# Kernel optimization log

Hardware: AMD Instinct MI355X
Metric: run time of the kernel (lower is better)

Reference implementation:

```python
import jax, jax.numpy as jnp
import numpy as np

D, H = 256, 4            # model dim, num heads
HD = D // H              # head dim (even, needed by rotate_half)
B, N, M, NS = 2, 6, 512, 512  # batch, views, t keypoints, s keypoints
EPS = 1e-5


def _linear(x, w, b):
    return x @ w + b


def _ln(x, g, b):
    mu = x.mean(-1, keepdims=True)
    var = ((x - mu) ** 2).mean(-1, keepdims=True)
    return (x - mu) * jax.lax.rsqrt(var + EPS) * g + b


def _ffn(x, f1w, f1b, lng, lnb, f2w, f2b):
    # Linear(2d,2d) -> LayerNorm -> exact GELU -> Linear(2d,d)
    h = jax.nn.gelu(_ln(_linear(x, f1w, f1b), lng, lnb), approximate=False)
    return _linear(h, f2w, f2b)


def _rotate_half(x):
    # pairs (x0,x1) -> (-x1, x0), interleaved
    return jnp.stack((-x[..., 1::2], x[..., 0::2]), axis=-1).reshape(x.shape)


def _rope(freqs, t):
    return t * freqs[0] + _rotate_half(t) * freqs[1]


def _attn(q, k, v):
    sim = jnp.einsum('...id,...jd->...ij', q, k) * (q.shape[-1] ** -0.5)
    return jnp.einsum('...ij,...jd->...id', jax.nn.softmax(sim, axis=-1), v)


def _self_block(x, enc, qkv_w, qkv_b, out_w, out_b, *ffn_p):
    b, n_img, m, d = x.shape
    enc = jnp.swapaxes(enc, 2, 3)  # encoding.dim()==6 path
    qkv = _linear(x, qkv_w, qkv_b).reshape(b, n_img, m, H, HD, 3)
    qkv = jnp.swapaxes(qkv, -4, -3)  # [b,N,H,m,hd,3]
    q, k, v = qkv[..., 0], qkv[..., 1], qkv[..., 2]
    ctx = _attn(_rope(enc, q), _rope(enc, k), v)  # [b,N,H,m,hd]
    msg = _linear(jnp.swapaxes(ctx, -3, -2).reshape(b, n_img, m, d), out_w, out_b)
    return x + _ffn(jnp.concatenate([x, msg], -1), *ffn_p)


def _t2t_block(t, qkv_w, qkv_b, out_w, out_b, *ffn_p):
    t2 = jnp.swapaxes(t, 1, 2)  # [b,m,N,d]
    b, m, n_img, d = t2.shape
    qkv = _linear(t2, qkv_w, qkv_b).reshape(b, m, n_img, H, HD, 3)
    qkv = jnp.swapaxes(qkv, 3, 2)  # [b,m,H,N,hd,3]
    q, k, v = qkv[..., 0], qkv[..., 1], qkv[..., 2]
    ctx = _attn(q, k, v)  # [b,m,H,N,hd]
    msg = _linear(jnp.swapaxes(ctx, 3, 2).reshape(b, m, n_img, d), out_w, out_b)
    return jnp.swapaxes(t2 + _ffn(jnp.concatenate([t2, msg], -1), *ffn_p), 1, 2)


def _s2s_block(s, q_enc, k_enc, qkv_w, qkv_b, out_w, out_b, *ffn_p):
    b, n_img, n, d = s.shape
    qkv = _linear(s, qkv_w, qkv_b).reshape(b, n_img, n, H, HD, 3)
    qkv = jnp.swapaxes(jnp.swapaxes(qkv, -4, -3), -5, -4)  # [b,H,N,n,hd,3]
    q, k, v = qkv[..., 0], qkv[..., 1], qkv[..., 2]
    # expand queries across all views, RoPE per (i,j) view pair
    q = jnp.broadcast_to(q[:, :, None], (b, H, n_img, n_img, n, HD))
    q = _rope(q_enc, q).reshape(b, H, n_img, n_img * n, HD)
    k = _rope(k_enc, k)
    ctx = _attn(q, k, v).reshape(b, H, n_img, n_img, n, HD)
    # drop diagonal (i==j) entries exactly like boolean-mask indexing in torch
    off = np.nonzero(~np.eye(n_img, dtype=bool).ravel())[0]
    ctx = ctx.reshape(b, H, n_img * n_img, n, HD)[:, :, off]
    ctx = ctx.reshape(b, H, n_img - 1, n_img, n, HD).mean(2)  # [b,H,N,n,hd]
    ctx = jnp.swapaxes(jnp.swapaxes(ctx, 1, 2), 2, 3).reshape(b, n_img, n, d)
    msg = _linear(ctx, out_w, out_b)
    return s + _ffn(jnp.concatenate([s, msg], -1), *ffn_p)


def _cross_block(d0, d1, q_w, q_b, kv_w, kv_b, out_w, out_b, *ffn_p):
    b, n_img, m, d = d0.shape
    m1 = d1.shape[2]
    q = jnp.swapaxes(_linear(d0, q_w, q_b).reshape(b, n_img, m, H, HD), 2, 3)
    kv = jnp.swapaxes(_linear(d1, kv_w, kv_b).reshape(b, n_img, m1, H, HD, 2), 2, 3)
    ctx = _attn(q, kv[..., 0], kv[..., 1])  # [b,N,H,m,hd]
    msg = _linear(jnp.swapaxes(ctx, 2, 3).reshape(b, n_img, m, d), out_w, out_b)
    return d0 + _ffn(jnp.concatenate([d0, msg], -1), *ffn_p)


def setup_inputs() -> dict:
    key = jax.random.key(0)
    ks = iter(jax.random.split(key, 80))
    f32 = jnp.float32

    def lin(din, dout):
        return (jax.random.normal(next(ks), (din, dout), f32) * (din ** -0.5),
                jnp.zeros((dout,), f32))

    inp = {}
    inp['t_desc'] = jax.random.normal(next(ks), (B, N, M, D), f32)
    inp['s_desc'] = jax.random.normal(next(ks), (B, N, NS, D), f32)
    inp['t_encoding'] = jax.random.normal(next(ks), (2, 1, 1, N, M, HD), f32)
    inp['s_encoding'] = jax.random.normal(next(ks), (2, 1, 1, N, NS, HD), f32)
    inp['q_encoding'] = jax.random.normal(next(ks), (2, 1, 1, N, N, 1, HD), f32)
    inp['k_encoding'] = jax.random.normal(next(ks), (2, 1, 1, N, NS, HD), f32)
    for pre in ('sa', 'ss', 'tt'):
        inp[pre + '_qkv_w'], inp[pre + '_qkv_b'] = lin(D, 3 * D)
        inp[pre + '_out_w'], inp[pre + '_out_b'] = lin(D, D)
        inp[pre + '_f1_w'], inp[pre + '_f1_b'] = lin(2 * D, 2 * D)
        inp[pre + '_ln_g'] = jnp.ones((2 * D,), f32)
        inp[pre + '_ln_b'] = jnp.zeros((2 * D,), f32)
        inp[pre + '_f2_w'], inp[pre + '_f2_b'] = lin(2 * D, D)
    inp['ca_q_w'], inp['ca_q_b'] = lin(D, D)
    inp['ca_kv_w'], inp['ca_kv_b'] = lin(D, 2 * D)
    inp['ca_out_w'], inp['ca_out_b'] = lin(D, D)
    inp['ca_f1_w'], inp['ca_f1_b'] = lin(2 * D, 2 * D)
    inp['ca_ln_g'] = jnp.ones((2 * D,), f32)
    inp['ca_ln_b'] = jnp.zeros((2 * D,), f32)
    inp['ca_f2_w'], inp['ca_f2_b'] = lin(2 * D, D)
    inp['cf_w1'], inp['cf_b1'] = lin(D, D)
    inp['cf_w2'], inp['cf_b2'] = lin(D, 1)
    return inp


def reference(t_desc, s_desc, t_encoding, s_encoding, q_encoding, k_encoding,
              sa_qkv_w, sa_qkv_b, sa_out_w, sa_out_b, sa_f1_w, sa_f1_b, sa_ln_g, sa_ln_b, sa_f2_w, sa_f2_b,
              ss_qkv_w, ss_qkv_b, ss_out_w, ss_out_b, ss_f1_w, ss_f1_b, ss_ln_g, ss_ln_b, ss_f2_w, ss_f2_b,
              tt_qkv_w, tt_qkv_b, tt_out_w, tt_out_b, tt_f1_w, tt_f1_b, tt_ln_g, tt_ln_b, tt_f2_w, tt_f2_b,
              ca_q_w, ca_q_b, ca_kv_w, ca_kv_b, ca_out_w, ca_out_b, ca_f1_w, ca_f1_b, ca_ln_g, ca_ln_b, ca_f2_w, ca_f2_b,
              cf_w1, cf_b1, cf_w2, cf_b2):
    sa = (sa_qkv_w, sa_qkv_b, sa_out_w, sa_out_b, sa_f1_w, sa_f1_b, sa_ln_g, sa_ln_b, sa_f2_w, sa_f2_b)
    t = _self_block(t_desc, t_encoding, *sa)   # shared SelfBlock weights
    s = _self_block(s_desc, s_encoding, *sa)
    t = _t2t_block(t, tt_qkv_w, tt_qkv_b, tt_out_w, tt_out_b, tt_f1_w, tt_f1_b, tt_ln_g, tt_ln_b, tt_f2_w, tt_f2_b)
    s = _s2s_block(s, q_encoding, k_encoding, ss_qkv_w, ss_qkv_b, ss_out_w, ss_out_b, ss_f1_w, ss_f1_b, ss_ln_g, ss_ln_b, ss_f2_w, ss_f2_b)
    ca = (ca_q_w, ca_q_b, ca_kv_w, ca_kv_b, ca_out_w, ca_out_b, ca_f1_w, ca_f1_b, ca_ln_g, ca_ln_b, ca_f2_w, ca_f2_b)
    t2 = _cross_block(t, s, *ca)               # shared CrossBlock weights
    s2 = _cross_block(s, t, *ca)
    conf = _linear(jax.nn.relu(_linear(jax.lax.stop_gradient(s), cf_w1, cf_b1)), cf_w2, cf_b2)[..., 0]
    return t2, s2, conf
```

## Files before the change

### kernel.cpp

```cpp
#include <hip/hip_runtime.h>
#include <hip/hip_bf16.h>
#include <math.h>

constexpr int kD   = 256;
constexpr int kH   = 4;
constexpr int kHD  = 64;
constexpr int kB   = 2;
constexpr int kN   = 6;
constexpr int kM   = 512;
constexpr int kRowsH = kB*kN*kM;
constexpr int kRows  = 2*kRowsH;
constexpr int kGrpH  = kB*kN*kH;
constexpr int kGrp   = 2*kGrpH;
constexpr size_t kTOK = (size_t)kRowsH*kD;
constexpr size_t kEncSlab = (size_t)kN*kM*kHD;
constexpr size_t kQEncSlab = (size_t)kN*kN*kHD;
constexpr float kL2E = 1.4426950408889634f;

typedef unsigned short u16;
typedef __attribute__((ext_vector_type(8))) short s16x8;
typedef __attribute__((ext_vector_type(4))) float f32x4;

__device__ __forceinline__ float wred_sum(float v){
  #pragma unroll
  for (int m=32;m>0;m>>=1) v += __shfl_xor(v, m, 64);
  return v;
}
__device__ __forceinline__ u16 f2b(float x){
  union { float f; unsigned u; } a; a.f = x;
  unsigned r = a.u + 0x7fffu + ((a.u >> 16) & 1u);
  return (u16)(r >> 16);
}
__device__ __forceinline__ float b2f(u16 x){
  union { unsigned u; float f; } a; a.u = ((unsigned)x) << 16;
  return a.f;
}
__device__ __forceinline__ unsigned pk2(float lo, float hi){
  union { __hip_bfloat162 h2; unsigned u; } c;
  c.h2 = __float22bfloat162_rn(make_float2(lo, hi));
  return c.u;
}

struct WtDesc { const float* W; u16* Wt; int K; int N; int ntiles; };
struct WtTable { WtDesc d[18]; };

__global__ __launch_bounds__(256) void wtcast_k(WtTable tab)
{
  int t = blockIdx.x, mi = 0;
  while (t >= tab.d[mi].ntiles) { t -= tab.d[mi].ntiles; ++mi; }
  const float* W = tab.d[mi].W;
  u16* Wt = tab.d[mi].Wt;
  const int K = tab.d[mi].K, N = tab.d[mi].N;
  const int ktn = K >> 5;
  const int nt = t / ktn, kt = t % ktn;
  const int n0 = nt*128, k0 = kt*32;
  u16* dst = Wt + (size_t)t*4096;
  #pragma unroll
  for (int s = 0; s < 2; ++s) {
    const int idx0 = (s*256 + (int)threadIdx.x)*8;
    const int ar = idx0 >> 5;
    const int w8 = (idx0 >> 3) & 3;
    const int sw = (ar >> 1) & 3;
    const int kk = k0 + ((w8 ^ sw) << 3);
    const int n  = n0 + ar;
    union { u16 u[8]; s16x8 v; } o;
    #pragma unroll
    for (int e = 0; e < 8; ++e)
      o.u[e] = f2b(W[(size_t)(kk + e)*N + n]);
    *(s16x8*)(dst + idx0) = o.v;
  }
}

template<bool A1B, bool A2B, bool CB>
__global__ __launch_bounds__(256) void mmad_k(
    const void* __restrict__ A1a, const void* __restrict__ A1b,
    const void* __restrict__ A2a, const void* __restrict__ A2b, int K1,
    const u16* __restrict__ Wa, const u16* __restrict__ Wb,
    const float* __restrict__ bia, const float* __restrict__ bib,
    const float* __restrict__ bi2a, const float* __restrict__ bi2b, int Ns,
    const float* __restrict__ Ra, const float* __restrict__ Rb,
    void* __restrict__ Cp, int N, int K, int Mh, int doRelu)
{
  __shared__ u16 As[128*32];
  __shared__ u16 Bs[128*32];
  const int tid = threadIdx.x;
  const int lane = tid & 63, w = tid >> 6;
  const int gx = gridDim.x;
  const int nblk = gx * gridDim.y;
  int flat = blockIdx.y*gx + blockIdx.x;
  if (!(nblk & 7)) flat = (flat & 7)*(nblk >> 3) + (flat >> 3);
  const int bxx = flat % gx, byy = flat / gx;
  const int row0 = byy*128, col0 = bxx*128;
  const bool sec = (row0 >= Mh);
  const int lr0 = sec ? row0 - Mh : row0;
  const void* A1 = sec ? A1b : A1a;
  const void* A2 = sec ? A2b : A2a;
  const u16* Wt  = sec ? Wb : Wa;
  const float* bias  = sec ? bib : bia;
  const float* bias2 = sec ? bi2b : bi2a;
  const float* R = sec ? Rb : Ra;
  const int wr = (w >> 1)*64, wc = (w & 1)*64;
// ... 140 lines not shown
    vs[il][c] = base[c*3+2];
  }
  __syncthreads();
  #pragma unroll 4
  for (int rr = 0; rr < 16; ++rr) {
    const int cc = rr*4 + t4;
    Vt[((size_t)g*kHD + cc)*kM + i0 + c] = vs[c][cc];
  }
}

__global__ __launch_bounds__(256) void prep_cross_k(
    const u16* __restrict__ qkvC, u16* __restrict__ Kb, u16* __restrict__ Vt)
{
  __shared__ u16 vs[64][66];
  const int g = blockIdx.x >> 3, i0 = (blockIdx.x & 7)*64;
  const int h = g & 3, bn = g >> 2;
  const int src = (bn < 12) ? bn + 12 : bn - 12;
  const int c = threadIdx.x & 63, t4 = threadIdx.x >> 6;
  #pragma unroll 4
  for (int rr = 0; rr < 16; ++rr) {
    const int il = rr*4 + t4, i = i0 + il;
    const u16* base = qkvC + ((size_t)src*kM + i)*768 + 256 + h*128;
    Kb[((size_t)g*kM + i)*kHD + c] = f2b(b2f(base[c*2]) * 0.125f);
    vs[il][c] = base[c*2+1];
  }
  __syncthreads();
  #pragma unroll 4
  for (int rr = 0; rr < 16; ++rr) {
    const int cc = rr*4 + t4;
    Vt[((size_t)g*kHD + cc)*kM + i0 + c] = vs[c][cc];
  }
}

__device__ __forceinline__ f32x4 vmax4(f32x4 a, f32x4 b){
  f32x4 r;
  r[0]=fmaxf(a[0],b[0]); r[1]=fmaxf(a[1],b[1]);
  r[2]=fmaxf(a[2],b[2]); r[3]=fmaxf(a[3],b[3]);
  return r;
}

__device__ __forceinline__ void attn_seg(
    const u16* __restrict__ Kg, const u16* __restrict__ Vg,
    s16x8 qf0, s16x8 qf1, int k0, int qr, int hi,
    f32x4 acc[4], float& m, float& l, bool first)
{
  const bool subhi = (hi & 1);
  const bool up = (hi >= 2);
  f32x4 st[16];
  #pragma unroll
  for (int t2 = 0; t2 < 16; ++t2) {
    const u16* kp = Kg + ((size_t)(k0 + t2*16 + qr))*kHD + hi*8;
    s16x8 a0 = *(const s16x8*)(kp);
    s16x8 a1 = *(const s16x8*)(kp + 32);
    f32x4 z = {0.f, 0.f, 0.f, 0.f};
    z = __builtin_amdgcn_mfma_f32_16x16x32_bf16(a0, qf0, z, 0, 0, 0);
    z = __builtin_amdgcn_mfma_f32_16x16x32_bf16(a1, qf1, z, 0, 0, 0);
    st[t2] = z;
  }
  f32x4 t8[8];
  #pragma unroll
  for (int i = 0; i < 8; ++i) t8[i] = vmax4(st[2*i], st[2*i+1]);
  #pragma unroll
  for (int i = 0; i < 4; ++i) t8[i] = vmax4(t8[i], t8[i+4]);
  t8[0] = vmax4(vmax4(t8[0], t8[1]), vmax4(t8[2], t8[3]));
  float mloc = fmaxf(fmaxf(t8[0][0], t8[0][1]), fmaxf(t8[0][2], t8[0][3]));
  mloc = fmaxf(mloc, __shfl_xor(mloc, 16));
  mloc = fmaxf(mloc, __shfl_xor(mloc, 32));
  if (first) {
    m = mloc;
  } else if (__any(mloc > m)) {
    const float mn = fmaxf(m, mloc);
    const float r = exp2f((m - mn)*kL2E);
    m = mn;
    l *= r;
    const float rr0 = __shfl(r, hi*4+0), rr1 = __shfl(r, hi*4+1);
    const float rr2 = __shfl(r, hi*4+2), rr3 = __shfl(r, hi*4+3);
    #pragma unroll
    for (int db = 0; db < 4; ++db) {
      acc[db][0] *= rr0; acc[db][1] *= rr1; acc[db][2] *= rr2; acc[db][3] *= rr3;
    }
  }
  const float mk = m * kL2E;
  #pragma unroll
  for (int t2 = 0; t2 < 16; ++t2)
    #pragma unroll
    for (int i = 0; i < 4; ++i)
      st[t2][i] = exp2f(st[t2][i]*kL2E - mk);
  {
    f32x4 s8[8];
    #pragma unroll
    for (int i = 0; i < 8; ++i) s8[i] = st[2*i] + st[2*i+1];
    #pragma unroll
    for (int i = 0; i < 4; ++i) s8[i] = s8[i] + s8[i+4];
    f32x4 s1 = (s8[0] + s8[1]) + (s8[2] + s8[3]);
    l += (s1[0] + s1[1]) + (s1[2] + s1[3]);
  }
  #pragma unroll
  for (int j = 0; j < 8; ++j) {
    const unsigned c00 = pk2(st[2*j][0],   st[2*j][1]);
    const unsigned c01 = pk2(st[2*j][2],   st[2*j][3]);
    const unsigned c10 = pk2(st[2*j+1][0], st[2*j+1][1]);
    const unsigned c11 = pk2(st[2*j+1][2], st[2*j+1][3]);
    const unsigned c00x = __shfl_xor((int)c00, 32), c10x = __shfl_xor((int)c10, 32);
    const unsigned c01x = __shfl_xor((int)c01, 32), c11x = __shfl_xor((int)c11, 32);
    const unsigned E = up ? c10x : c00, F = up ? c10 : c00x;
    const unsigned G = up ? c11x : c01, H = up ? c11 : c01x;
    const unsigned Ex = __shfl_xor((int)E, 16), Fx = __shfl_xor((int)F, 16);
    const unsigned Gx = __shfl_xor((int)G, 16), Hx = __shfl_xor((int)H, 16);
    union { unsigned w[4]; s16x8 v; } pa;
    pa.w[0] = subhi ? Fx : E;
    pa.w[1] = subhi ? Hx : G;
    pa.w[2] = subhi ? F  : Ex;
    pa.w[3] = subhi ? H  : Gx;
    #pragma unroll
    for (int db = 0; db < 4; ++db) {
      const u16* vp = Vg + ((size_t)(db*16 + qr))*kM + k0 + j*32 + hi*8;
      const s16x8 vf = *(const s16x8*)(vp);
      acc[db] = __builtin_amdgcn_mfma_f32_16x16x32_bf16(pa.v, vf, acc[db], 0, 0, 0);
    }
  }
}

__device__ __forceinline__ void attn_512(
    const u16* __restrict__ Kg, const u16* __restrict__ Vg,
    s16x8 qf0, s16x8 qf1, int qr, int hi, f32x4 acc[4], float& m, float& l)
{
  attn_seg(Kg, Vg, qf0, qf1, 0,   qr, hi, acc, m, l, true);
  attn_seg(Kg, Vg, qf0, qf1, 256, qr, hi, acc, m, l, false);
}

template<int CROSSQ>
__global__ __launch_bounds__(256) void attn_mm_k(
    const u16* __restrict__ Qb, const u16* __restrict__ Kb,
    const u16* __restrict__ Vt, u16* __restrict__ ctx)
{
  const int w = threadIdx.x >> 6, lane = threadIdx.x & 63;
  const int bij = (blockIdx.x & 7)*96 + (blockIdx.x >> 3);
  const int g = bij >> 3, qblk = bij & 7;
  const int h = g & 3, bn = g >> 2;
  const int q0 = qblk*64 + w*16;
  const int qr = lane & 15, hi = lane >> 4;

  s16x8 qf0, qf1;
  if (CROSSQ) {
    const u16* qp = Qb + ((size_t)(bn*kM + q0 + qr))*768 + h*kHD + hi*8;
    qf0 = *(const s16x8*)(qp); qf1 = *(const s16x8*)(qp + 32);
  } else {
    const u16* qp = Qb + ((size_t)g*kM + q0 + qr)*kHD + hi*8;
    qf0 = *(const s16x8*)(qp); qf1 = *(const s16x8*)(qp + 32);
  }

  const u16* Kg = Kb + (size_t)g*kM*kHD;
  const u16* Vg = Vt + (size_t)g*kHD*kM;
  f32x4 acc[4] = {};
  float m = -1e30f, l = 0.f;
  attn_512(Kg, Vg, qf0, qf1, qr, hi, acc, m, l);

  l += __shfl_xor(l, 16); l += __shfl_xor(l, 32);
  const float li = 1.f/l;
  const float l0 = __shfl(li, hi*4+0), l1 = __shfl(li, hi*4+1);
  const float l2 = __shfl(li, hi*4+2), l3 = __shfl(li, hi*4+3);
  #pragma unroll
  for (int db = 0; db < 4; ++db) {
    const size_t base = ((size_t)(bn*kM + q0 + hi*4))*kD + h*kHD + db*16 + qr;
    ctx[base + 0*kD] = f2b(acc[db][0]*l0);
    ctx[base + 1*kD] = f2b(acc[db][1]*l1);
    ctx[base + 2*kD] = f2b(acc[db][2]*l2);
    ctx[base + 3*kD] = f2b(acc[db][3]*l3);
  }
}

__device__ __forceinline__ void rope4(const f32x4 x, const f32x4 e0, const f32x4 e1, float o[4])
{
  o[0] = x[0]*e0[0] - x[1]*e1[0];
  o[1] = x[1]*e0[1] + x[0]*e1[1];
  o[2] = x[2]*e0[2] - x[3]*e1[2];
  o[3] = x[3]*e0[3] + x[2]*e1[3];
}

__global__ __launch_bounds__(256) void attn_s2s_k(
    const float* __restrict__ Qraw, const u16* __restrict__ Kb,
    const u16* __restrict__ Vt, const float* __restrict__ qenc,
    u16* __restrict__ ctx5)
{
  const int w = threadIdx.x >> 6, lane = threadIdx.x & 63;
  const int bij = (blockIdx.x & 7)*120 + (blockIdx.x >> 3);
  const int bh = bij / 120;
  const int rest = bij % 120;
  const int col = rest / 20;
  const int rem = rest % 20;
  const int qblk = rem / 5, split = rem % 5;
  const int q0 = qblk*128 + w*32;
  const int qr = lane & 15, hi = lane >> 4;
  const bool subhi = (hi & 1), up = (hi >= 2);

  const int e  = split*6 + col;
  const int iv = e/5;
  const int j0 = e%5;
  const int jv = j0 + (j0 >= iv ? 1 : 0);

  s16x8 qf0[2], qf1[2];
  #pragma unroll
  for (int f = 0; f < 2; ++f) {
    const float* qp = Qraw + ((size_t)(bh*kN + jv)*kM + q0 + f*16 + qr)*kHD + hi*8;
    const float* ep = qenc + ((size_t)(iv*kN + jv))*kHD + hi*8;
    union { u16 u[8]; s16x8 v; } A, B;
    float o[4];
    rope4(*(const f32x4*)(qp),   *(const f32x4*)(ep),   *(const f32x4*)(ep+kQEncSlab), o);
    #pragma unroll
    for (int j = 0; j < 4; ++j) A.u[j] = f2b(o[j]*0.125f);
    rope4(*(const f32x4*)(qp+4), *(const f32x4*)(ep+4), *(const f32x4*)(ep+kQEncSlab+4), o);
    #pragma unroll
    for (int j = 0; j < 4; ++j) A.u[4+j] = f2b(o[j]*0.125f);
    rope4(*(const f32x4*)(qp+32), *(const f32x4*)(ep+32), *(const f32x4*)(ep+kQEncSlab+32), o);
    #pragma unroll
    for (int j = 0; j < 4; ++j) B.u[j] = f2b(o[j]*0.125f);
    rope4(*(const f32x4*)(qp+36), *(const f32x4*)(ep+36), *(const f32x4*)(ep+kQEncSlab+36), o);
    #pragma unroll
    for (int j = 0; j < 4; ++j) B.u[4+j] = f2b(o[j]*0.125f);
    qf0[f] = A.v; qf1[f] = B.v;
  }

  const int g2 = bh*kN + iv;
  const u16* Kg = Kb + (size_t)g2*kM*kHD;
  const u16* Vg = Vt + (size_t)g2*kHD*kM;
  f32x4 acc[2][4] = {};
  float m[2] = {-1e30f, -1e30f}, l[2] = {0.f, 0.f};

  for (int kc = 0; kc < 16; ++kc) {
    const int k0 = kc*32;
    s16x8 a0[2], a1[2];
    #pragma unroll
    for (int t = 0; t < 2; ++t) {
      const u16* kp = Kg + ((size_t)(k0 + t*16 + qr))*kHD + hi*8;
      a0[t] = *(const s16x8*)(kp);
      a1[t] = *(const s16x8*)(kp + 32);
    }
    s16x8 pa[2];
    #pragma unroll
    for (int f = 0; f < 2; ++f) {
      f32x4 st[2];
      #pragma unroll
      for (int t = 0; t < 2; ++t) {
        f32x4 z = {0.f, 0.f, 0.f, 0.f};
        z = __builtin_amdgcn_mfma_f32_16x16x32_bf16(a0[t], qf0[f], z, 0, 0, 0);
        z = __builtin_amdgcn_mfma_f32_16x16x32_bf16(a1[t], qf1[f], z, 0, 0, 0);
        st[t] = z;
      }
      float mloc = fmaxf(fmaxf(fmaxf(st[0][0], st[0][1]), fmaxf(st[0][2], st[0][3])),
                         fmaxf(fmaxf(st[1][0], st[1][1]), fmaxf(st[1][2], st[1][3])));
      mloc = fmaxf(mloc, __shfl_xor(mloc, 16));
      mloc = fmaxf(mloc, __shfl_xor(mloc, 32));
      if (!__all(mloc - m[f] <= 8.f)) {
        const float mn = fmaxf(m[f], mloc);
        const float r = exp2f((m[f] - mn)*kL2E);
        m[f] = mn;
        l[f] *= r;
        const float rr0 = __shfl(r, hi*4+0), rr1 = __shfl(r, hi*4+1);
// ... 9 lines not shown
      for (int t = 0; t < 2; ++t)
        #pragma unroll
        for (int j = 0; j < 4; ++j) {
          const float pv = exp2f((st[t][j] - m[f])*kL2E);
          p[t*4+j] = pv; ls += pv;
        }
      l[f] += ls;
      const unsigned c00 = pk2(p[0], p[1]);
      const unsigned c01 = pk2(p[2], p[3]);
      const unsigned c10 = pk2(p[4], p[5]);
      const unsigned c11 = pk2(p[6], p[7]);
      const unsigned c00x = __shfl_xor((int)c00, 32), c10x = __shfl_xor((int)c10, 32);
      const unsigned c01x = __shfl_xor((int)c01, 32), c11x = __shfl_xor((int)c11, 32);
      const unsigned E = up ? c10x : c00, F = up ? c10 : c00x;
      const unsigned G = up ? c11x : c01, H = up ? c11 : c01x;
      const unsigned Ex = __shfl_xor((int)E, 16), Fx = __shfl_xor((int)F, 16);
      const unsigned Gx = __shfl_xor((int)G, 16), Hx = __shfl_xor((int)H, 16);
      union { unsigned w[4]; s16x8 v; } pw;
      pw.w[0] = subhi ? Fx : E;
      pw.w[1] = subhi ? Hx : G;
      pw.w[2] = subhi ? F  : Ex;
      pw.w[3] = subhi ? H  : Gx;
      pa[f] = pw.v;
    }
    #pragma unroll
    for (int db = 0; db < 4; ++db) {
      const u16* vp = Vg + ((size_t)(db*16 + qr))*kM + k0 + hi*8;
      const s16x8 vf = *(const s16x8*)(vp);
      acc[0][db] = __builtin_amdgcn_mfma_f32_16x16x32_bf16(pa[0], vf, acc[0][db], 0, 0, 0);
      acc[1][db] = __builtin_amdgcn_mfma_f32_16x16x32_bf16(pa[1], vf, acc[1][db], 0, 0, 0);
    }
  }

  const int b = bh >> 2, h = bh & 3;
  u16* outp = ctx5 + (size_t)split*kTOK;
  #pragma unroll
  for (int f = 0; f < 2; ++f) {
    float lf = l[f];
    lf += __shfl_xor(lf, 16); lf += __shfl_xor(lf, 32);
    const float li = 0.2f/lf;
    const float l0 = __shfl(li, hi*4+0), l1 = __shfl(li, hi*4+1);
    const float l2 = __shfl(li, hi*4+2), l3 = __shfl(li, hi*4+3);
    #pragma unroll
    for (int db = 0; db < 4; ++db) {
      const size_t base = ((size_t)((b*kN + col)*kM + q0 + f*16 + hi*4))*kD + h*kHD + db*16 + qr;
      outp[base + 0*kD] = f2b(acc[f][db][0]*l0);
      outp[base + 1*kD] = f2b(acc[f][db][1]*l1);
      outp[base + 2*kD] = f2b(acc[f][db][2]*l2);
      outp[base + 3*kD] = f2b(acc[f][db][3]*l3);
    }
  }
}

__global__ __launch_bounds__(256) void sum5_k(const u16* __restrict__ c5,
                                              u16* __restrict__ outU)
{
  const size_t i4 = ((size_t)blockIdx.x*256 + threadIdx.x)*4;
  float s0=0.f, s1=0.f, s2=0.f, s3=0.f;
  #pragma unroll
  for (int sp = 0; sp < 5; ++sp) {
    uint2 d = *(const uint2*)(c5 + sp*kTOK + i4);
    s0 += b2f((u16)(d.x & 0xffff)); s1 += b2f((u16)(d.x >> 16));
    s2 += b2f((u16)(d.y & 0xffff)); s3 += b2f((u16)(d.y >> 16));
  }
  union { u16 u[4]; uint2 d; } o;
  o.u[0]=f2b(s0); o.u[1]=f2b(s1); o.u[2]=f2b(s2); o.u[3]=f2b(s3);
// ... 67 lines not shown
  float s = 0.f;
  #pragma unroll
  for (int j=0;j<4;++j) s = fmaf(t[lane+j*64], w2[lane+j*64], s);
  s = wred_sum(s);
  if (lane == 0) out[row] = s + b2[0];
}

extern "C" void kernel_launch(void* const* d_in, const int* in_sizes, int n_in,
                              void* d_out, int out_size, void* d_ws, size_t ws_size,
                              hipStream_t stream)
{
  auto F = [&](int i){ return (const float*)d_in[i]; };
  const float* t_desc = F(0);
  const float* s_desc = F(1);
  const float* t_enc  = F(2);
  const float* s_enc  = F(3);
  const float* q_enc  = F(4);
  const float* k_enc  = F(5);

  char* base = (char*)d_ws;
  float* xts = (float*)base;
  float* xt = xts;
  float* xs = xts + kTOK;
  char* R1  = base + 2*kTOK*sizeof(float);
  char* CTX = R1 + 4*kTOK*sizeof(float);
  char* MSG = CTX + 2*kTOK*sizeof(u16);
  u16* Qb16 = (u16*)(MSG + kTOK*sizeof(float));
  u16* Kb16 = Qb16 + 2*kTOK;
  u16* Vt16 = Kb16 + 2*kTOK;
  u16* wsW  = Vt16 + 2*kTOK;
  u16*   qkvU  = (u16*)R1;
  float* hbuf  = (float*)R1;
  u16*   ctx5  = (u16*)R1;
  u16*   ctxU  = (u16*)CTX;
  u16*   msgU  = (u16*)MSG;
  float* Qs2s  = (float*)MSG;
  float* confb = (float*)MSG;
  u16*   yU    = (u16*)CTX;

  float* out_t2s2 = (float*)d_out;
  float* out_conf = (float*)d_out + 2*kTOK;

  WtTable tab;
  int nd = 0, total_tiles = 0;
  size_t woff = 0;
  const u16* wp[18];
  auto addw = [&](int idx, int K, int N){
    u16* dst = wsW + woff;
    tab.d[nd] = { F(idx), dst, K, N, (N>>7)*(K>>5) };
    total_tiles += tab.d[nd].ntiles;
    wp[nd] = dst;
    woff += (size_t)K*N;
    ++nd;
    return nd-1;
  };
  const int W_SA_QKV = addw(6, 256, 768);
  const int W_SA_OUT = addw(8, 256, 256);
  const int W_SA_F1  = addw(10, 512, 512);
  const int W_SA_F2  = addw(14, 512, 256);
  const int W_SS_QKV = addw(16, 256, 768);
  const int W_SS_OUT = addw(18, 256, 256);
  const int W_SS_F1  = addw(20, 512, 512);
  const int W_SS_F2  = addw(24, 512, 256);
  const int W_TT_QKV = addw(26, 256, 768);
  const int W_TT_OUT = addw(28, 256, 256);
  const int W_TT_F1  = addw(30, 512, 512);
  const int W_TT_F2  = addw(34, 512, 256);
  const int W_CA_Q   = addw(36, 256, 256);
  const int W_CA_KV  = addw(38, 256, 512);
  const int W_CA_OUT = addw(40, 256, 256);
  const int W_CA_F1  = addw(42, 512, 512);
  const int W_CA_F2  = addw(46, 512, 256);
  const int W_CF_1   = addw(48, 256, 256);
  (void)W_CA_KV;
  wtcast_k<<<total_tiles, 256, 0, stream>>>(tab);

  auto mm_f32_to_b16 = [&](const float* a1a, const float* a1b, int wa, int wb2,
                           const float* ba, const float* bb2, u16* c, int N_, int K_){
    dim3 grid(N_/128, kRows/128);
    mmad_k<false,false,true><<<grid,256,0,stream>>>(a1a, a1b, nullptr, nullptr, K_,
        wp[wa], wp[wb2], ba, bb2, ba, bb2, N_, nullptr, nullptr, c, N_, K_, kRowsH, 0);
  };
  auto mm_b16_to_b16 = [&](const u16* a1a, const u16* a1b, int wa, int wb2,
                           const float* ba, const float* bb2, u16* c, int N_, int K_){
    dim3 grid(N_/128, kRows/128);
    mmad_k<true,false,true><<<grid,256,0,stream>>>(a1a, a1b, nullptr, nullptr, K_,
        wp[wa], wp[wb2], ba, bb2, ba, bb2, N_, nullptr, nullptr, c, N_, K_, kRowsH, 0);
  };
  auto mm_f1 = [&](const float* a1a, const float* a1b, const u16* a2a, const u16* a2b,
                   int wa, int wb2, const float* ba, const float* bb2, float* c){
    dim3 grid(512/128, kRows/128);
    mmad_k<false,true,false><<<grid,256,0,stream>>>(a1a, a1b, a2a, a2b, 256,
        wp[wa], wp[wb2], ba, bb2, ba, bb2, 512, nullptr, nullptr, c, 512, 512, kRowsH, 0);
  };
  auto mm_f2 = [&](const u16* a1a, const u16* a1b, int wa, int wb2,
                   const float* ba, const float* bb2,
                   const float* ra, const float* rb, float* c){
    dim3 grid(256/128, kRows/128);
    mmad_k<true,false,false><<<grid,256,0,stream>>>(a1a, a1b, nullptr, nullptr, 512,
        wp[wa], wp[wb2], ba, bb2, ba, bb2, 256, ra, rb, c, 256, 512, kRowsH, 0);
  };

  mm_f32_to_b16(t_desc, s_desc, W_SA_QKV, W_SA_QKV, F(7), F(7), qkvU, 768, 256);
  prep_self_k<<<kGrp*8, 256, 0, stream>>>(qkvU, t_enc, s_enc, Qb16, Kb16, Vt16);
  attn_mm_k<0><<<kGrp*8, 256, 0, stream>>>(Qb16, Kb16, Vt16, ctxU);
  mm_b16_to_b16(ctxU, ctxU + kTOK, W_SA_OUT, W_SA_OUT, F(9), F(9), msgU, 256, 256);
  mm_f1(t_desc, s_desc, msgU, msgU + kTOK, W_SA_F1, W_SA_F1, F(11), F(11), hbuf);
  lngelu_k<<<kRows, 256, 0, stream>>>(hbuf, yU, F(12), F(13), F(12), F(13), kRowsH);
  mm_f2(yU, yU + (size_t)kRowsH*512, W_SA_F2, W_SA_F2, F(15), F(15), t_desc, s_desc, xts);

  mm_f32_to_b16(xt, xs, W_TT_QKV, W_SS_QKV, F(27), F(17), qkvU, 768, 256);
  prep_s2s_k<<<kGrpH*8, 256, 0, stream>>>(qkvU, k_enc, Qs2s, Kb16, Vt16);
  attn_t2t_k<<<(kB*kH*kN*kM)/4, 256, 0, stream>>>(qkvU, ctxU);
  attn_s2s_k<<<960, 256, 0, stream>>>(Qs2s, Kb16, Vt16, q_enc, ctx5);
  sum5_k<<<(int)(kTOK/1024), 256, 0, stream>>>(ctx5, ctxU + kTOK);
  mm_b16_to_b16(ctxU, ctxU + kTOK, W_TT_OUT, W_SS_OUT, F(29), F(19), msgU, 256, 256);
  mm_f1(xt, xs, msgU, msgU + kTOK, W_TT_F1, W_SS_F1, F(31), F(21), hbuf);
  lngelu_k<<<kRows, 256, 0, stream>>>(hbuf, yU, F(32), F(33), F(22), F(23), kRowsH);
  mm_f2(yU, yU + (size_t)kRowsH*512, W_TT_F2, W_SS_F2, F(35), F(25), xt, xs, xts);

  {
    dim3 grid(2, kRowsH/128);
    mmad_k<false,false,false><<<grid,256,0,stream>>>(xs, xs, nullptr, nullptr, 256,
        wp[W_CF_1], wp[W_CF_1], F(49), F(49), F(49), F(49), 256,
        nullptr, nullptr, confb, 256, 256, kRowsH, 1);
  }
  conf_dot_k<<<kRowsH/4, 256, 0, stream>>>(confb, F(50), F(51), out_conf);

  {
    dim3 grid(768/128, kRows/128);
    mmad_k<false,false,true><<<grid,256,0,stream>>>(xt, xs, nullptr, nullptr, 256,
        wp[W_CA_Q], wp[W_CA_Q], F(37), F(37), F(39), F(39), 256,
        nullptr, nullptr, qkvU, 768, 256, kRowsH, 0);
  }
  prep_cross_k<<<kGrp*8, 256, 0, stream>>>(qkvU, Kb16, Vt16);
  attn_mm_k<1><<<kGrp*8, 256, 0, stream>>>(qkvU, Kb16, Vt16, ctxU);
  mm_b16_to_b16(ctxU, ctxU + kTOK, W_CA_OUT, W_CA_OUT, F(41), F(41), msgU, 256, 256);
  mm_f1(xt, xs, msgU, msgU + kTOK, W_CA_F1, W_CA_F1, F(43), F(43), hbuf);
  lngelu_k<<<kRows, 256, 0, stream>>>(hbuf, yU, F(44), F(45), F(44), F(45), kRowsH);
  mm_f2(yU, yU + (size_t)kRowsH*512, W_CA_F2, W_CA_F2, F(47), F(47), xt, xs, out_t2s2);
}
```

Before: 523.8 us.

## Fold attention out-projection into FFN first linear and widen attention query tiles

```diff
diff --git a/kernel.cpp b/kernel.cpp
--- a/kernel.cpp
+++ b/kernel.cpp
@@ -41,7 +41,66 @@
   return c.u;
 }
 
-struct WtDesc { const float* W; u16* Wt; int K; int N; int ntiles; };
+struct FuseArgs {
+  const float* Wout[4]; const float* W1[4];
+  const float* bout[4]; const float* b1[4];
+  float* Wtmp; float* b1p;
+};
+
+__global__ __launch_bounds__(256) void wfuse_k(FuseArgs fa)
+{
+  const int set = blockIdx.x >> 5;
+  const int t = blockIdx.x & 31;
+  const int row0 = (t >> 3)*64, col0 = (t & 7)*64;
+  const float* A  = fa.Wout[set];
+  const float* Bm = fa.W1[set] + 256*512;
+  float* C = fa.Wtmp + (size_t)set*(256*512);
+  __shared__ float As[16][65];
+  __shared__ float Bs[16][64];
+  const int tid = threadIdx.x;
+  const int tx = tid & 15, ty = tid >> 4;
+  const int ar = tid >> 2, ak = (tid & 3)*4;
+  const int wr = tid >> 4, wc = (tid & 15)*4;
+  float acc[4][4] = {};
+  for (int kt = 0; kt < 256; kt += 16) {
+    float4 av = *(const float4*)(A + (size_t)(row0+ar)*256 + kt + ak);
+    As[ak+0][ar]=av.x; As[ak+1][ar]=av.y; As[ak+2][ar]=av.z; As[ak+3][ar]=av.w;
+    *(float4*)(&Bs[wr][wc]) = *(const float4*)(Bm + (size_t)(kt+wr)*512 + col0 + wc);
+    __syncthreads();
+    #pragma unroll
+    for (int k2=0;k2<16;++k2) {
+      float a[4], b[4];
+      #pragma unroll
+      for (int i=0;i<4;++i) a[i]=As[k2][ty*4+i];
+      #pragma unroll
+      for (int j=0;j<4;++j) b[j]=Bs[k2][tx*4+j];
+      #pragma unroll
+      for (int i=0;i<4;++i)
+        #pragma unroll
+        for (int j=0;j<4;++j) acc[i][j] = fmaf(a[i], b[j], acc[i][j]);
+    }
+    __syncthreads();
+  }
+  #pragma unroll
+  for (int i=0;i<4;++i)
+    #pragma unroll
+    for (int j=0;j<4;++j)
+      C[(size_t)(row0+ty*4+i)*512 + col0+tx*4+j] = acc[i][j];
+}
+
+__global__ __launch_bounds__(256) void biasfuse_k(FuseArgs fa)
+{
+  const int set = blockIdx.x >> 1;
+  const int n = (blockIdx.x & 1)*256 + threadIdx.x;
+  const float* W1 = fa.W1[set];
+  const float* bo = fa.bout[set];
+  float s = fa.b1[set][n];
+  for (int k = 0; k < 256; ++k)
+    s = fmaf(bo[k], W1[(size_t)(256+k)*512 + n], s);
+  fa.b1p[set*512 + n] = s;
+}
+
+struct WtDesc { const float* W; const float* W2; u16* Wt; int K; int N; int ntiles; };
 struct WtTable { WtDesc d[18]; };
 
 __global__ __launch_bounds__(256) void wtcast_k(WtTable tab)
@@ -49,6 +108,7 @@
   int t = blockIdx.x, mi = 0;
   while (t >= tab.d[mi].ntiles) { t -= tab.d[mi].ntiles; ++mi; }
   const float* W = tab.d[mi].W;
+  const float* W2 = tab.d[mi].W2;
   u16* Wt = tab.d[mi].Wt;
   const int K = tab.d[mi].K, N = tab.d[mi].N;
   const int ktn = K >> 5;
@@ -61,12 +121,14 @@
     const int ar = idx0 >> 5;
     const int w8 = (idx0 >> 3) & 3;
     const int sw = (ar >> 1) & 3;
-    const int kk = k0 + ((w8 ^ sw) << 3);
+    int kk = k0 + ((w8 ^ sw) << 3);
     const int n  = n0 + ar;
+    const float* src = W;
+    if (W2 && kk >= 256) { src = W2; kk -= 256; }
     union { u16 u[8]; s16x8 v; } o;
     #pragma unroll
     for (int e = 0; e < 8; ++e)
-      o.u[e] = f2b(W[(size_t)(kk + e)*N + n]);
+      o.u[e] = f2b(src[(size_t)(kk + e)*N + n]);
     *(s16x8*)(dst + idx0) = o.v;
   }
 }
@@ -273,198 +335,31 @@
   }
 }
 
-__device__ __forceinline__ f32x4 vmax4(f32x4 a, f32x4 b){
-  f32x4 r;
-  r[0]=fmaxf(a[0],b[0]); r[1]=fmaxf(a[1],b[1]);
-  r[2]=fmaxf(a[2],b[2]); r[3]=fmaxf(a[3],b[3]);
-  return r;
-}
-
-__device__ __forceinline__ void attn_seg(
-    const u16* __restrict__ Kg, const u16* __restrict__ Vg,
-    s16x8 qf0, s16x8 qf1, int k0, int qr, int hi,
-    f32x4 acc[4], float& m, float& l, bool first)
-{
-  const bool subhi = (hi & 1);
-  const bool up = (hi >= 2);
-  f32x4 st[16];
-  #pragma unroll
-  for (int t2 = 0; t2 < 16; ++t2) {
-    const u16* kp = Kg + ((size_t)(k0 + t2*16 + qr))*kHD + hi*8;
-    s16x8 a0 = *(const s16x8*)(kp);
-    s16x8 a1 = *(const s16x8*)(kp + 32);
-    f32x4 z = {0.f, 0.f, 0.f, 0.f};
-    z = __builtin_amdgcn_mfma_f32_16x16x32_bf16(a0, qf0, z, 0, 0, 0);
-    z = __builtin_amdgcn_mfma_f32_16x16x32_bf16(a1, qf1, z, 0, 0, 0);
-    st[t2] = z;
-  }
-  f32x4 t8[8];
-  #pragma unroll
-  for (int i = 0; i < 8; ++i) t8[i] = vmax4(st[2*i], st[2*i+1]);
-  #pragma unroll
-  for (int i = 0; i < 4; ++i) t8[i] = vmax4(t8[i], t8[i+4]);
-  t8[0] = vmax4(vmax4(t8[0], t8[1]), vmax4(t8[2], t8[3]));
-  float mloc = fmaxf(fmaxf(t8[0][0], t8[0][1]), fmaxf(t8[0][2], t8[0][3]));
-  mloc = fmaxf(mloc, __shfl_xor(mloc, 16));
-  mloc = fmaxf(mloc, __shfl_xor(mloc, 32));
-  if (first) {
-    m = mloc;
-  } else if (__any(mloc > m)) {
-    const float mn = fmaxf(m, mloc);
-    const float r = exp2f((m - mn)*kL2E);
-    m = mn;
-    l *= r;
-    const float rr0 = __shfl(r, hi*4+0), rr1 = __shfl(r, hi*4+1);
-    const float rr2 = __shfl(r, hi*4+2), rr3 = __shfl(r, hi*4+3);
-    #pragma unroll
-    for (int db = 0; db < 4; ++db) {
-      acc[db][0] *= rr0; acc[db][1] *= rr1; acc[db][2] *= rr2; acc[db][3] *= rr3;
-    }
-  }
-  const float mk = m * kL2E;
-  #pragma unroll
-  for (int t2 = 0; t2 < 16; ++t2)
-    #pragma unroll
-    for (int i = 0; i < 4; ++i)
-      st[t2][i] = exp2f(st[t2][i]*kL2E - mk);
-  {
-    f32x4 s8[8];
-    #pragma unroll
-    for (int i = 0; i < 8; ++i) s8[i] = st[2*i] + st[2*i+1];
-    #pragma unroll
-    for (int i = 0; i < 4; ++i) s8[i] = s8[i] + s8[i+4];
-    f32x4 s1 = (s8[0] + s8[1]) + (s8[2] + s8[3]);
-    l += (s1[0] + s1[1]) + (s1[2] + s1[3]);
-  }
-  #pragma unroll
-  for (int j = 0; j < 8; ++j) {
-    const unsigned c00 = pk2(st[2*j][0],   st[2*j][1]);
-    const unsigned c01 = pk2(st[2*j][2],   st[2*j][3]);
-    const unsigned c10 = pk2(st[2*j+1][0], st[2*j+1][1]);
-    const unsigned c11 = pk2(st[2*j+1][2], st[2*j+1][3]);
-    const unsigned c00x = __shfl_xor((int)c00, 32), c10x = __shfl_xor((int)c10, 32);
-    const unsigned c01x = __shfl_xor((int)c01, 32), c11x = __shfl_xor((int)c11, 32);
-    const unsigned E = up ? c10x : c00, F = up ? c10 : c00x;
-    const unsigned G = up ? c11x : c01, H = up ? c11 : c01x;
-    const unsigned Ex = __shfl_xor((int)E, 16), Fx = __shfl_xor((int)F, 16);
-    const unsigned Gx = __shfl_xor((int)G, 16), Hx = __shfl_xor((int)H, 16);
-    union { unsigned w[4]; s16x8 v; } pa;
-    pa.w[0] = subhi ? Fx : E;
-    pa.w[1] = subhi ? Hx : G;
-    pa.w[2] = subhi ? F  : Ex;
-    pa.w[3] = subhi ? H  : Gx;
-    #pragma unroll
-    for (int db = 0; db < 4; ++db) {
-      const u16* vp = Vg + ((size_t)(db*16 + qr))*kM + k0 + j*32 + hi*8;
-      const s16x8 vf = *(const s16x8*)(vp);
-      acc[db] = __builtin_amdgcn_mfma_f32_16x16x32_bf16(pa.v, vf, acc[db], 0, 0, 0);
-    }
-  }
-}
-
-__device__ __forceinline__ void attn_512(
-    const u16* __restrict__ Kg, const u16* __restrict__ Vg,
-    s16x8 qf0, s16x8 qf1, int qr, int hi, f32x4 acc[4], float& m, float& l)
-{
-  attn_seg(Kg, Vg, qf0, qf1, 0,   qr, hi, acc, m, l, true);
-  attn_seg(Kg, Vg, qf0, qf1, 256, qr, hi, acc, m, l, false);
-}
-
 template<int CROSSQ>
 __global__ __launch_bounds__(256) void attn_mm_k(
     const u16* __restrict__ Qb, const u16* __restrict__ Kb,
     const u16* __restrict__ Vt, u16* __restrict__ ctx)
 {
   const int w = threadIdx.x >> 6, lane = threadIdx.x & 63;
-  const int bij = (blockIdx.x & 7)*96 + (blockIdx.x >> 3);
-  const int g = bij >> 3, qblk = bij & 7;
+  const int bij = (blockIdx.x & 7)*48 + (blockIdx.x >> 3);
+  const int g = bij >> 2, qblk = bij & 3;
   const int h = g & 3, bn = g >> 2;
-  const int q0 = qblk*64 + w*16;
-  const int qr = lane & 15, hi = lane >> 4;
-
-  s16x8 qf0, qf1;
-  if (CROSSQ) {
-    const u16* qp = Qb + ((size_t)(bn*kM + q0 + qr))*768 + h*kHD + hi*8;
-    qf0 = *(const s16x8*)(qp); qf1 = *(const s16x8*)(qp + 32);
-  } else {
-    const u16* qp = Qb + ((size_t)g*kM + q0 + qr)*kHD + hi*8;
-    qf0 = *(const s16x8*)(qp); qf1 = *(const s16x8*)(qp + 32);
-  }
-
-  const u16* Kg = Kb + (size_t)g*kM*kHD;
-  const u16* Vg = Vt + (size_t)g*kHD*kM;
-  f32x4 acc[4] = {};
-  float m = -1e30f, l = 0.f;
-  attn_512(Kg, Vg, qf0, qf1, qr, hi, acc, m, l);
-
-  l += __shfl_xor(l, 16); l += __shfl_xor(l, 32);
-  const float li = 1.f/l;
-  const float l0 = __shfl(li, hi*4+0), l1 = __shfl(li, hi*4+1);
-  const float l2 = __shfl(li, hi*4+2), l3 = __shfl(li, hi*4+3);
-  #pragma unroll
-  for (int db = 0; db < 4; ++db) {
-    const size_t base = ((size_t)(bn*kM + q0 + hi*4))*kD + h*kHD + db*16 + qr;
-    ctx[base + 0*kD] = f2b(acc[db][0]*l0);
-    ctx[base + 1*kD] = f2b(acc[db][1]*l1);
-    ctx[base + 2*kD] = f2b(acc[db][2]*l2);
-    ctx[base + 3*kD] = f2b(acc[db][3]*l3);
-  }
-}
-
-__device__ __forceinline__ void rope4(const f32x4 x, const f32x4 e0, const f32x4 e1, float o[4])
-{
-  o[0] = x[0]*e0[0] - x[1]*e1[0];
-  o[1] = x[1]*e0[1] + x[0]*e1[1];
-  o[2] = x[2]*e0[2] - x[3]*e1[2];
-  o[3] = x[3]*e0[3] + x[2]*e1[3];
-}
-
-__global__ __launch_bounds__(256) void attn_s2s_k(
-    const float* __restrict__ Qraw, const u16* __restrict__ Kb,
-    const u16* __restrict__ Vt, const float* __restrict__ qenc,
-    u16* __restrict__ ctx5)
-{
-  const int w = threadIdx.x >> 6, lane = threadIdx.x & 63;
-  const int bij = (blockIdx.x & 7)*120 + (blockIdx.x >> 3);
-  const int bh = bij / 120;
-  const int rest = bij % 120;
-  const int col = rest / 20;
-  const int rem = rest % 20;
-  const int qblk = rem / 5, split = rem % 5;
   const int q0 = qblk*128 + w*32;
   const int qr = lane & 15, hi = lane >> 4;
   const bool subhi = (hi & 1), up = (hi >= 2);
 
-  const int e  = split*6 + col;
-  const int iv = e/5;
-  const int j0 = e%5;
-  const int jv = j0 + (j0 >= iv ? 1 : 0);
-
   s16x8 qf0[2], qf1[2];
   #pragma unroll
   for (int f = 0; f < 2; ++f) {
-    const float* qp = Qraw + ((size_t)(bh*kN + jv)*kM + q0 + f*16 + qr)*kHD + hi*8;
-    const float* ep = qenc + ((size_t)(iv*kN + jv))*kHD + hi*8;
-    union { u16 u[8]; s16x8 v; } A, B;
-    float o[4];
-    rope4(*(const f32x4*)(qp),   *(const f32x4*)(ep),   *(const f32x4*)(ep+kQEncSlab), o);
-    #pragma unroll
-    for (int j = 0; j < 4; ++j) A.u[j] = f2b(o[j]*0.125f);
-    rope4(*(const f32x4*)(qp+4), *(const f32x4*)(ep+4), *(const f32x4*)(ep+kQEncSlab+4), o);
-    #pragma unroll
-    for (int j = 0; j < 4; ++j) A.u[4+j] = f2b(o[j]*0.125f);
-    rope4(*(const f32x4*)(qp+32), *(const f32x4*)(ep+32), *(const f32x4*)(ep+kQEncSlab+32), o);
-    #pragma unroll
-    for (int j = 0; j < 4; ++j) B.u[j] = f2b(o[j]*0.125f);
-    rope4(*(const f32x4*)(qp+36), *(const f32x4*)(ep+36), *(const f32x4*)(ep+kQEncSlab+36), o);
-    #pragma unroll
-    for (int j = 0; j < 4; ++j) B.u[4+j] = f2b(o[j]*0.125f);
-    qf0[f] = A.v; qf1[f] = B.v;
-  }
-
-  const int g2 = bh*kN + iv;
-  const u16* Kg = Kb + (size_t)g2*kM*kHD;
-  const u16* Vg = Vt + (size_t)g2*kHD*kM;
+    const u16* qp = CROSSQ
+      ? Qb + ((size_t)(bn*kM + q0 + f*16 + qr))*768 + h*kHD + hi*8
+      : Qb + ((size_t)g*kM + q0 + f*16 + qr)*kHD + hi*8;
+    qf0[f] = *(const s16x8*)(qp);
+    qf1[f] = *(const s16x8*)(qp + 32);
+  }
+
+  const u16* Kg = Kb + (size_t)g*kM*kHD;
+  const u16* Vg = Vt + (size_t)g*kHD*kM;
   f32x4 acc[2][4] = {};
   float m[2] = {-1e30f, -1e30f}, l[2] = {0.f, 0.f};
 
@@ -540,6 +435,153 @@
     }
   }
 
+  #pragma unroll
+  for (int f = 0; f < 2; ++f) {
+    float lf = l[f];
+    lf += __shfl_xor(lf, 16); lf += __shfl_xor(lf, 32);
+    const float li = 1.f/lf;
+    const float l0 = __shfl(li, hi*4+0), l1 = __shfl(li, hi*4+1);
+    const float l2 = __shfl(li, hi*4+2), l3 = __shfl(li, hi*4+3);
+    #pragma unroll
+    for (int db = 0; db < 4; ++db) {
+      const size_t base = ((size_t)(bn*kM + q0 + f*16 + hi*4))*kD + h*kHD + db*16 + qr;
+      ctx[base + 0*kD] = f2b(acc[f][db][0]*l0);
+      ctx[base + 1*kD] = f2b(acc[f][db][1]*l1);
+      ctx[base + 2*kD] = f2b(acc[f][db][2]*l2);
+      ctx[base + 3*kD] = f2b(acc[f][db][3]*l3);
+    }
+  }
+}
+
+__device__ __forceinline__ void rope4(const f32x4 x, const f32x4 e0, const f32x4 e1, float o[4])
+{
+  o[0] = x[0]*e0[0] - x[1]*e1[0];
+  o[1] = x[1]*e0[1] + x[0]*e1[1];
+  o[2] = x[2]*e0[2] - x[3]*e1[2];
+  o[3] = x[3]*e0[3] + x[2]*e1[3];
+}
+
+__global__ __launch_bounds__(256) void attn_s2s_k(
+    const float* __restrict__ Qraw, const u16* __restrict__ Kb,
+    const u16* __restrict__ Vt, const float* __restrict__ qenc,
+    u16* __restrict__ ctx5)
+{
+  const int w = threadIdx.x >> 6, lane = threadIdx.x & 63;
+  const int bij = (blockIdx.x & 7)*120 + (blockIdx.x >> 3);
+  const int bh = bij / 120;
+  const int rest = bij % 120;
+  const int col = rest / 20;
+  const int rem = rest % 20;
+  const int qblk = rem / 5, split = rem % 5;
+  const int q0 = qblk*128 + w*32;
+  const int qr = lane & 15, hi = lane >> 4;
+  const bool subhi = (hi & 1), up = (hi >= 2);
+
+  const int e  = split*6 + col;
+  const int iv = e/5;
+  const int j0 = e%5;
+  const int jv = j0 + (j0 >= iv ? 1 : 0);
+
+  s16x8 qf0[2], qf1[2];
+  #pragma unroll
+  for (int f = 0; f < 2; ++f) {
+    const float* qp = Qraw + ((size_t)(bh*kN + jv)*kM + q0 + f*16 + qr)*kHD + hi*8;
+    const float* ep = qenc + ((size_t)(iv*kN + jv))*kHD + hi*8;
+    union { u16 u[8]; s16x8 v; } A, B;
+    float o[4];
+    rope4(*(const f32x4*)(qp),   *(const f32x4*)(ep),   *(const f32x4*)(ep+kQEncSlab), o);
+    #pragma unroll
+    for (int j = 0; j < 4; ++j) A.u[j] = f2b(o[j]*0.125f);
+    rope4(*(const f32x4*)(qp+4), *(const f32x4*)(ep+4), *(const f32x4*)(ep+kQEncSlab+4), o);
+    #pragma unroll
+    for (int j = 0; j < 4; ++j) A.u[4+j] = f2b(o[j]*0.125f);
+    rope4(*(const f32x4*)(qp+32), *(const f32x4*)(ep+32), *(const f32x4*)(ep+kQEncSlab+32), o);
+    #pragma unroll
+    for (int j = 0; j < 4; ++j) B.u[j] = f2b(o[j]*0.125f);
+    rope4(*(const f32x4*)(qp+36), *(const f32x4*)(ep+36), *(const f32x4*)(ep+kQEncSlab+36), o);
+    #pragma unroll
+    for (int j = 0; j < 4; ++j) B.u[4+j] = f2b(o[j]*0.125f);
+    qf0[f] = A.v; qf1[f] = B.v;
+  }
+
+  const int g2 = bh*kN + iv;
+  const u16* Kg = Kb + (size_t)g2*kM*kHD;
+  const u16* Vg = Vt + (size_t)g2*kHD*kM;
+  f32x4 acc[2][4] = {};
+  float m[2] = {-1e30f, -1e30f}, l[2] = {0.f, 0.f};
+
+  for (int kc = 0; kc < 16; ++kc) {
+    const int k0 = kc*32;
+    s16x8 a0[2], a1[2];
+    #pragma unroll
+    for (int t = 0; t < 2; ++t) {
+      const u16* kp = Kg + ((size_t)(k0 + t*16 + qr))*kHD + hi*8;
+      a0[t] = *(const s16x8*)(kp);
+      a1[t] = *(const s16x8*)(kp + 32);
+    }
+    s16x8 pa[2];
+    #pragma unroll
+    for (int f = 0; f < 2; ++f) {
+      f32x4 st[2];
+      #pragma unroll
+      for (int t = 0; t < 2; ++t) {
+        f32x4 z = {0.f, 0.f, 0.f, 0.f};
+        z = __builtin_amdgcn_mfma_f32_16x16x32_bf16(a0[t], qf0[f], z, 0, 0, 0);
+        z = __builtin_amdgcn_mfma_f32_16x16x32_bf16(a1[t], qf1[f], z, 0, 0, 0);
+        st[t] = z;
+      }
+      float mloc = fmaxf(fmaxf(fmaxf(st[0][0], st[0][1]), fmaxf(st[0][2], st[0][3])),
+                         fmaxf(fmaxf(st[1][0], st[1][1]), fmaxf(st[1][2], st[1][3])));
+      mloc = fmaxf(mloc, __shfl_xor(mloc, 16));
+      mloc = fmaxf(mloc, __shfl_xor(mloc, 32));
+      if (!__all(mloc - m[f] <= 8.f)) {
+        const float mn = fmaxf(m[f], mloc);
+        const float r = exp2f((m[f] - mn)*kL2E);
+        m[f] = mn;
+        l[f] *= r;
+        const float rr0 = __shfl(r, hi*4+0), rr1 = __shfl(r, hi*4+1);
+        const float rr2 = __shfl(r, hi*4+2), rr3 = __shfl(r, hi*4+3);
+        #pragma unroll
+        for (int db = 0; db < 4; ++db) {
+          acc[f][db][0] *= rr0; acc[f][db][1] *= rr1;
+          acc[f][db][2] *= rr2; acc[f][db][3] *= rr3;
+        }
+      }
+      float p[8], ls = 0.f;
+      #pragma unroll
+      for (int t = 0; t < 2; ++t)
+        #pragma unroll
+        for (int j = 0; j < 4; ++j) {
+          const float pv = exp2f((st[t][j] - m[f])*kL2E);
+          p[t*4+j] = pv; ls += pv;
+        }
+      l[f] += ls;
+      const unsigned c00 = pk2(p[0], p[1]);
+      const unsigned c01 = pk2(p[2], p[3]);
+      const unsigned c10 = pk2(p[4], p[5]);
+      const unsigned c11 = pk2(p[6], p[7]);
+      const unsigned c00x = __shfl_xor((int)c00, 32), c10x = __shfl_xor((int)c10, 32);
+      const unsigned c01x = __shfl_xor((int)c01, 32), c11x = __shfl_xor((int)c11, 32);
+      const unsigned E = up ? c10x : c00, F = up ? c10 : c00x;
+      const unsigned G = up ? c11x : c01, H = up ? c11 : c01x;
+      const unsigned Ex = __shfl_xor((int)E, 16), Fx = __shfl_xor((int)F, 16);
+      const unsigned Gx = __shfl_xor((int)G, 16), Hx = __shfl_xor((int)H, 16);
+      union { unsigned w[4]; s16x8 v; } pw;
+      pw.w[0] = subhi ? Fx : E;
+      pw.w[1] = subhi ? Hx : G;
+      pw.w[2] = subhi ? F  : Ex;
+      pw.w[3] = subhi ? H  : Gx;
+      pa[f] = pw.v;
+    }
+    #pragma unroll
+    for (int db = 0; db < 4; ++db) {
+      const u16* vp = Vg + ((size_t)(db*16 + qr))*kM + k0 + hi*8;
+      const s16x8 vf = *(const s16x8*)(vp);
+      acc[0][db] = __builtin_amdgcn_mfma_f32_16x16x32_bf16(pa[0], vf, acc[0][db], 0, 0, 0);
+      acc[1][db] = __builtin_amdgcn_mfma_f32_16x16x32_bf16(pa[1], vf, acc[1][db], 0, 0, 0);
+    }
+  }
+
   const int b = bh >> 2, h = bh & 3;
   u16* outp = ctx5 + (size_t)split*kTOK;
   #pragma unroll
@@ -673,8 +715,8 @@
   u16*   qkvU  = (u16*)R1;
   float* hbuf  = (float*)R1;
   u16*   ctx5  = (u16*)R1;
+  float* Wtmp  = (float*)R1;
   u16*   ctxU  = (u16*)CTX;
-  u16*   msgU  = (u16*)MSG;
   float* Qs2s  = (float*)MSG;
   float* confb = (float*)MSG;
   u16*   yU    = (u16*)CTX;
@@ -686,46 +728,46 @@
   int nd = 0, total_tiles = 0;
   size_t woff = 0;
   const u16* wp[18];
-  auto addw = [&](int idx, int K, int N){
+  auto addw = [&](int idx, const float* W2, int K, int N){
     u16* dst = wsW + woff;
-    tab.d[nd] = { F(idx), dst, K, N, (N>>7)*(K>>5) };
+    tab.d[nd] = { F(idx), W2, dst, K, N, (N>>7)*(K>>5) };
     total_tiles += tab.d[nd].ntiles;
     wp[nd] = dst;
     woff += (size_t)K*N;
     ++nd;
     return nd-1;
   };
-  const int W_SA_QKV = addw(6, 256, 768);
-  const int W_SA_OUT = addw(8, 256, 256);
-  const int W_SA_F1  = addw(10, 512, 512);
-  const int W_SA_F2  = addw(14, 512, 256);
-  const int W_SS_QKV = addw(16, 256, 768);
-  const int W_SS_OUT = addw(18, 256, 256);
-  const int W_SS_F1  = addw(20, 512, 512);
-  const int W_SS_F2  = addw(24, 512, 256);
-  const int W_TT_QKV = addw(26, 256, 768);
-  const int W_TT_OUT = addw(28, 256, 256);
-  const int W_TT_F1  = addw(30, 512, 512);
-  const int W_TT_F2  = addw(34, 512, 256);
-  const int W_CA_Q   = addw(36, 256, 256);
-  const int W_CA_KV  = addw(38, 256, 512);
-  const int W_CA_OUT = addw(40, 256, 256);
-  const int W_CA_F1  = addw(42, 512, 512);
-  const int W_CA_F2  = addw(46, 512, 256);
-  const int W_CF_1   = addw(48, 256, 256);
+  const int W_SA_QKV = addw(6,  nullptr, 256, 768);
+  const int W_SA_F1  = addw(10, Wtmp + 0*131072, 512, 512);
+  const int W_SA_F2  = addw(14, nullptr, 512, 256);
+  const int W_SS_QKV = addw(16, nullptr, 256, 768);
+  const int W_SS_F1  = addw(20, Wtmp + 1*131072, 512, 512);
+  const int W_SS_F2  = addw(24, nullptr, 512, 256);
+  const int W_TT_QKV = addw(26, nullptr, 256, 768);
+  const int W_TT_F1  = addw(30, Wtmp + 2*131072, 512, 512);
+  const int W_TT_F2  = addw(34, nullptr, 512, 256);
+  const int W_CA_Q   = addw(36, nullptr, 256, 256);
+  const int W_CA_KV  = addw(38, nullptr, 256, 512);
+  const int W_CA_F1  = addw(42, Wtmp + 3*131072, 512, 512);
+  const int W_CA_F2  = addw(46, nullptr, 512, 256);
+  const int W_CF_1   = addw(48, nullptr, 256, 256);
   (void)W_CA_KV;
+  float* b1p = (float*)(wsW + woff);
+
+  FuseArgs fa;
+  fa.Wout[0]=F(8);  fa.Wout[1]=F(18); fa.Wout[2]=F(28); fa.Wout[3]=F(40);
+  fa.W1[0]=F(10);   fa.W1[1]=F(20);   fa.W1[2]=F(30);   fa.W1[3]=F(42);
+  fa.bout[0]=F(9);  fa.bout[1]=F(19); fa.bout[2]=F(29); fa.bout[3]=F(41);
+  fa.b1[0]=F(11);   fa.b1[1]=F(21);   fa.b1[2]=F(31);   fa.b1[3]=F(43);
+  fa.Wtmp = Wtmp; fa.b1p = b1p;
+  wfuse_k<<<128, 256, 0, stream>>>(fa);
+  biasfuse_k<<<8, 256, 0, stream>>>(fa);
   wtcast_k<<<total_tiles, 256, 0, stream>>>(tab);
 
   auto mm_f32_to_b16 = [&](const float* a1a, const float* a1b, int wa, int wb2,
                            const float* ba, const float* bb2, u16* c, int N_, int K_){
     dim3 grid(N_/128, kRows/128);
     mmad_k<false,false,true><<<grid,256,0,stream>>>(a1a, a1b, nullptr, nullptr, K_,
-        wp[wa], wp[wb2], ba, bb2, ba, bb2, N_, nullptr, nullptr, c, N_, K_, kRowsH, 0);
-  };
-  auto mm_b16_to_b16 = [&](const u16* a1a, const u16* a1b, int wa, int wb2,
-                           const float* ba, const float* bb2, u16* c, int N_, int K_){
-    dim3 grid(N_/128, kRows/128);
-    mmad_k<true,false,true><<<grid,256,0,stream>>>(a1a, a1b, nullptr, nullptr, K_,
         wp[wa], wp[wb2], ba, bb2, ba, bb2, N_, nullptr, nullptr, c, N_, K_, kRowsH, 0);
   };
   auto mm_f1 = [&](const float* a1a, const float* a1b, const u16* a2a, const u16* a2b,
@@ -744,9 +786,8 @@
 
   mm_f32_to_b16(t_desc, s_desc, W_SA_QKV, W_SA_QKV, F(7), F(7), qkvU, 768, 256);
   prep_self_k<<<kGrp*8, 256, 0, stream>>>(qkvU, t_enc, s_enc, Qb16, Kb16, Vt16);
-  attn_mm_k<0><<<kGrp*8, 256, 0, stream>>>(Qb16, Kb16, Vt16, ctxU);
-  mm_b16_to_b16(ctxU, ctxU + kTOK, W_SA_OUT, W_SA_OUT, F(9), F(9), msgU, 256, 256);
-  mm_f1(t_desc, s_desc, msgU, msgU + kTOK, W_SA_F1, W_SA_F1, F(11), F(11), hbuf);
+  attn_mm_k<0><<<384, 256, 0, stream>>>(Qb16, Kb16, Vt16, ctxU);
+  mm_f1(t_desc, s_desc, ctxU, ctxU + kTOK, W_SA_F1, W_SA_F1, b1p+0*512, b1p+0*512, hbuf);
   lngelu_k<<<kRows, 256, 0, stream>>>(hbuf, yU, F(12), F(13), F(12), F(13), kRowsH);
   mm_f2(yU, yU + (size_t)kRowsH*512, W_SA_F2, W_SA_F2, F(15), F(15), t_desc, s_desc, xts);
 
@@ -755,8 +796,7 @@
   attn_t2t_k<<<(kB*kH*kN*kM)/4, 256, 0, stream>>>(qkvU, ctxU);
   attn_s2s_k<<<960, 256, 0, stream>>>(Qs2s, Kb16, Vt16, q_enc, ctx5);
   sum5_k<<<(int)(kTOK/1024), 256, 0, stream>>>(ctx5, ctxU + kTOK);
-  mm_b16_to_b16(ctxU, ctxU + kTOK, W_TT_OUT, W_SS_OUT, F(29), F(19), msgU, 256, 256);
-  mm_f1(xt, xs, msgU, msgU + kTOK, W_TT_F1, W_SS_F1, F(31), F(21), hbuf);
+  mm_f1(xt, xs, ctxU, ctxU + kTOK, W_TT_F1, W_SS_F1, b1p+2*512, b1p+1*512, hbuf);
   lngelu_k<<<kRows, 256, 0, stream>>>(hbuf, yU, F(32), F(33), F(22), F(23), kRowsH);
   mm_f2(yU, yU + (size_t)kRowsH*512, W_TT_F2, W_SS_F2, F(35), F(25), xt, xs, xts);
 
@@ -775,9 +815,8 @@
         nullptr, nullptr, qkvU, 768, 256, kRowsH, 0);
   }
   prep_cross_k<<<kGrp*8, 256, 0, stream>>>(qkvU, Kb16, Vt16);
-  attn_mm_k<1><<<kGrp*8, 256, 0, stream>>>(qkvU, Kb16, Vt16, ctxU);
-  mm_b16_to_b16(ctxU, ctxU + kTOK, W_CA_OUT, W_CA_OUT, F(41), F(41), msgU, 256, 256);
-  mm_f1(xt, xs, msgU, msgU + kTOK, W_CA_F1, W_CA_F1, F(43), F(43), hbuf);
+  attn_mm_k<1><<<384, 256, 0, stream>>>(qkvU, Kb16, Vt16, ctxU);
+  mm_f1(xt, xs, ctxU, ctxU + kTOK, W_CA_F1, W_CA_F1, b1p+3*512, b1p+3*512, hbuf);
   lngelu_k<<<kRows, 256, 0, stream>>>(hbuf, yU, F(44), F(45), F(44), F(45), kRowsH);
   mm_f2(yU, yU + (size_t)kRowsH*512, W_CA_F2, W_CA_F2, F(47), F(47), xt, xs, out_t2s2);
 }
```

New measurement: 483.6 us. -7.7%, faster.
